# Performance work log

Measured on AMD Instinct MI355X. Metric: run time of the kernel, lower is better.

Reference implementation:

```python
import jax, jax.numpy as jnp
import numpy as np

B = 65536

def setup_inputs() -> dict:
    key = jax.random.key(0)
    ks = jax.random.split(key, 6)
    x = jax.random.normal(ks[0], (B, 784), dtype=jnp.float32)
    w_conv = jnp.ones((3, 3), dtype=jnp.float32)  # Parameter(ones((3,3)))
    w1 = jax.random.normal(ks[1], (676, 256), dtype=jnp.float32) * 0.04
    b1 = jax.random.normal(ks[2], (256,), dtype=jnp.float32) * 0.01
    w2 = jax.random.normal(ks[3], (256, 10), dtype=jnp.float32) * 0.06
    b2 = jax.random.normal(ks[4], (10,), dtype=jnp.float32) * 0.01
    return {"x": x, "w_conv": w_conv, "w1": w1, "b1": b1, "w2": w2, "b2": b2}

def reference(x, w_conv, w1, b1, w2, b2):
    b = x.shape[0]
    img = x.reshape(b, 1, 28, 28)
    # Convolve() is cross-correlation (no kernel flip), 'VALID': 28->26
    kern = w_conv.reshape(1, 1, 3, 3)
    conv = jax.lax.conv_general_dilated(
        img, kern, window_strides=(1, 1), padding='VALID',
        dimension_numbers=('NCHW', 'OIHW', 'NCHW'))  # (B,1,26,26)
    feat = conv.reshape(b, 676)
    h = jax.nn.relu(feat @ w1 + b1)  # (B,256)
    return h @ w2 + b2               # (B,10)
```

## Files before the change

kernel.cpp:

```cpp
#include <hip/hip_runtime.h>
#include <hip/hip_bf16.h>
#include <stdint.h>

typedef __bf16 bf16;
typedef __attribute__((ext_vector_type(8))) __bf16 bf16x8;
typedef __attribute__((ext_vector_type(4))) float f32x4;

#define KREAL 784
#define NTILES 25
#define TROW   40
#define TILE_ELEMS (256 * TROW)

#define GLOBAL_AS __attribute__((address_space(1)))
#define LDS_AS    __attribute__((address_space(3)))

__global__ __launch_bounds__(256) void prep_w1tt(const float* __restrict__ w_conv,
                                                 const float* __restrict__ w1,
                                                 bf16* __restrict__ W) {
    const int tile = blockIdx.x / TROW;
    const int kk   = blockIdx.x % TROW;
    const int n    = threadIdx.x;
    const int k    = tile * 32 + kk;
    float s = 0.0f;
    if (kk < 32 && k < KREAL) {
        const int r = k / 28, c = k % 28;
        #pragma unroll
        for (int di = 0; di < 3; ++di) {
            const int i = r - di;
            if (i < 0 || i >= 26) continue;
            #pragma unroll
            for (int dj = 0; dj < 3; ++dj) {
                const int j = c - dj;
                if (j < 0 || j >= 26) continue;
                s += w_conv[di * 3 + dj] * w1[(i * 26 + j) * 256 + n];
            }
        }
    }
    W[(size_t)tile * TILE_ELEMS + n * TROW + kk] = (bf16)s;
}

__global__ __launch_bounds__(256, 2) void fused_mlp(
    const float* __restrict__ x,
    const bf16*  __restrict__ W,
    const float* __restrict__ b1,
    const float* __restrict__ w2,
    const float* __restrict__ b2,
    float* __restrict__ out)
{
    __shared__ bf16 Bs[3][TILE_ELEMS];

    const int t    = threadIdx.x;
    const int wave = t >> 6;
    const int lane = t & 63;
    const int c    = lane & 15;
    const int q    = lane >> 4;

    const int row0 = blockIdx.x * 128;

    const float* arow0 = x + (size_t)(row0 + wave * 32 + c) * KREAL + q * 8;
    const float* arow1 = arow0 + (size_t)16 * KREAL;
    const bf16* bsrc = W + (size_t)(wave * 5) * 512 + lane * 8;

    f32x4 acc[2][16];
    #pragma unroll
    for (int mt = 0; mt < 2; ++mt)
        #pragma unroll
        for (int nt = 0; nt < 16; ++nt)
            acc[mt][nt] = (f32x4){0.f, 0.f, 0.f, 0.f};

    float4 f0a = *(const float4*)arow0, f0b = *(const float4*)(arow0 + 4);
    float4 f1a = *(const float4*)arow1, f1b = *(const float4*)(arow1 + 4);
    #pragma unroll
    for (int j = 0; j < 5; ++j) {
        __builtin_amdgcn_global_load_lds(
            (const GLOBAL_AS void*)(bsrc + j * 512),
            (LDS_AS void*)((char*)&Bs[0][0] + (wave * 5 + j) * 1024), 16, 0, 0);
    }
    #pragma unroll
    for (int j = 0; j < 5; ++j) {
        __builtin_amdgcn_global_load_lds(
            (const GLOBAL_AS void*)(bsrc + TILE_ELEMS + j * 512),
            (LDS_AS void*)((char*)&Bs[1][0] + (wave * 5 + j) * 1024), 16, 0, 0);
    }
    bf16x8 a0, a1;
    a0[0] = (bf16)f0a.x; a0[1] = (bf16)f0a.y; a0[2] = (bf16)f0a.z; a0[3] = (bf16)f0a.w;
    a0[4] = (bf16)f0b.x; a0[5] = (bf16)f0b.y; a0[6] = (bf16)f0b.z; a0[7] = (bf16)f0b.w;
    a1[0] = (bf16)f1a.x; a1[1] = (bf16)f1a.y; a1[2] = (bf16)f1a.z; a1[3] = (bf16)f1a.w;
    a1[4] = (bf16)f1b.x; a1[5] = (bf16)f1b.y; a1[6] = (bf16)f1b.z; a1[7] = (bf16)f1b.w;

    asm volatile("s_waitcnt vmcnt(5)" ::: "memory");
    __builtin_amdgcn_sched_barrier(0);
    __builtin_amdgcn_s_barrier();
    __builtin_amdgcn_sched_barrier(0);

    #pragma unroll 1
    for (int it = 0; it < NTILES; ++it) {
        const int  cur   = it % 3;
        const bool more  = (it + 1) < NTILES;
        const bool more2 = (it + 2) < NTILES;

        float okm = 1.0f;
        if (more) {
            const int kn = (it + 1) * 32;
            const bool ok = (kn + q * 8) < KREAL;
            okm = ok ? 1.0f : 0.0f;
            const int koff = ok ? kn : 0;
            const float* p0 = arow0 + koff;
            const float* p1 = arow1 + koff;
            f0a = *(const float4*)p0; f0b = *(const float4*)(p0 + 4);
            f1a = *(const float4*)p1; f1b = *(const float4*)(p1 + 4);
        }

        if (more2) {
            const bf16* bs = bsrc + (size_t)(it + 2) * TILE_ELEMS;
            char* bd = (char*)&Bs[(it + 2) % 3][0] + wave * 5 * 1024;
            #pragma unroll
            for (int j = 0; j < 5; ++j) {
                __builtin_amdgcn_global_load_lds(
                    (const GLOBAL_AS void*)(bs + j * 512),
                    (LDS_AS void*)(bd + j * 1024), 16, 0, 0);
            }
        }

        {
            const bf16* bb = &Bs[cur][0] + c * TROW + q * 8;
            #pragma unroll
            for (int nt = 0; nt < 16; ++nt) {
                bf16x8 b = *(const bf16x8*)(bb + nt * 16 * TROW);
                acc[0][nt] = __builtin_amdgcn_mfma_f32_16x16x32_bf16(a0, b, acc[0][nt], 0, 0, 0);
                acc[1][nt] = __builtin_amdgcn_mfma_f32_16x16x32_bf16(a1, b, acc[1][nt], 0, 0, 0);
            }
        }

        if (more) {
            a0[0] = (bf16)(f0a.x * okm); a0[1] = (bf16)(f0a.y * okm);
            a0[2] = (bf16)(f0a.z * okm); a0[3] = (bf16)(f0a.w * okm);
            a0[4] = (bf16)(f0b.x * okm); a0[5] = (bf16)(f0b.y * okm);
            a0[6] = (bf16)(f0b.z * okm); a0[7] = (bf16)(f0b.w * okm);
            a1[0] = (bf16)(f1a.x * okm); a1[1] = (bf16)(f1a.y * okm);
            a1[2] = (bf16)(f1a.z * okm); a1[3] = (bf16)(f1a.w * okm);
            a1[4] = (bf16)(f1b.x * okm); a1[5] = (bf16)(f1b.y * okm);
            a1[6] = (bf16)(f1b.z * okm); a1[7] = (bf16)(f1b.w * okm);
        }

        if (more) {
            if (more2) {
                asm volatile("s_waitcnt vmcnt(5)" ::: "memory");
            } else {
                asm volatile("s_waitcnt vmcnt(0)" ::: "memory");
            }
            __builtin_amdgcn_sched_barrier(0);
            __builtin_amdgcn_s_barrier();
            __builtin_amdgcn_sched_barrier(0);
        }
    }

    float bl[16];
    #pragma unroll
    for (int nt = 0; nt < 16; ++nt) bl[nt] = b1[nt * 16 + c];

    #pragma unroll
    for (int mt = 0; mt < 2; ++mt)
        #pragma unroll
        for (int nt = 0; nt < 16; ++nt)
            #pragma unroll
            for (int r = 0; r < 4; ++r) {
                float v = acc[mt][nt][r] + bl[nt];
                acc[mt][nt][r] = v > 0.f ? v : 0.f;
            }

    #pragma unroll 1
    for (int j = 0; j < 10; ++j) {
        float wj[16];
        #pragma unroll
        for (int nt = 0; nt < 16; ++nt) wj[nt] = w2[(nt * 16 + c) * 10 + j];
        const float b2j = b2[j];
        #pragma unroll
        for (int mt = 0; mt < 2; ++mt)
            #pragma unroll
            for (int r = 0; r < 4; ++r) {
                float s = 0.f;
                #pragma unroll
                for (int nt = 0; nt < 16; ++nt) s += acc[mt][nt][r] * wj[nt];
                s += __shfl_xor(s, 1, 64);
                s += __shfl_xor(s, 2, 64);
                s += __shfl_xor(s, 4, 64);
                s += __shfl_xor(s, 8, 64);
                if (c == j) {
                    const int row = row0 + wave * 32 + mt * 16 + q * 4 + r;
                    out[(size_t)row * 10 + j] = s + b2j;
                }
            }
    }
}

extern "C" void kernel_launch(void* const* d_in, const int* in_sizes, int n_in,
                              void* d_out, int out_size, void* d_ws, size_t ws_size,
                              hipStream_t stream) {
    const float* x  = (const float*)d_in[0];
    const float* wc = (const float*)d_in[1];
    const float* w1 = (const float*)d_in[2];
    const float* b1 = (const float*)d_in[3];
    const float* w2 = (const float*)d_in[4];
    const float* b2 = (const float*)d_in[5];
    float* out = (float*)d_out;
    bf16* W = (bf16*)d_ws;

    prep_w1tt<<<dim3(NTILES * TROW), dim3(256), 0, stream>>>(wc, w1, W);
    fused_mlp<<<dim3(65536 / 128), dim3(256), 0, stream>>>(x, W, b1, w2, b2, out);
}
```

Before: 324.6 us.

## Halve rows per block and switch to double-buffered weight tiles for occupancy

Each wave now computes 16 rows instead of 32, so the block tile shrinks from 128 to 64 rows and the grid doubles. The weight staging in LDS drops from triple to double buffering, with a full vmcnt(0) wait each iteration. Launch bounds rise to 4 blocks per SM, aiming to hide x-load latency through occupancy. The cost is that each weight tile read from LDS and global memory now feeds half as many MFMAs, and prefetch depth is reduced.

```diff
diff --git a/kernel.cpp b/kernel.cpp
--- a/kernel.cpp
+++ b/kernel.cpp
@@ -39,7 +39,7 @@
     W[(size_t)tile * TILE_ELEMS + n * TROW + kk] = (bf16)s;
 }
 
-__global__ __launch_bounds__(256, 2) void fused_mlp(
+__global__ __launch_bounds__(256, 4) void fused_mlp(
     const float* __restrict__ x,
     const bf16*  __restrict__ W,
     const float* __restrict__ b1,
@@ -47,7 +47,7 @@
     const float* __restrict__ b2,
     float* __restrict__ out)
 {
-    __shared__ bf16 Bs[3][TILE_ELEMS];
+    __shared__ bf16 Bs[2][TILE_ELEMS];
 
     const int t    = threadIdx.x;
     const int wave = t >> 6;
@@ -55,49 +55,36 @@
     const int c    = lane & 15;
     const int q    = lane >> 4;
 
-    const int row0 = blockIdx.x * 128;
+    const int row0 = blockIdx.x * 64;
 
-    const float* arow0 = x + (size_t)(row0 + wave * 32 + c) * KREAL + q * 8;
-    const float* arow1 = arow0 + (size_t)16 * KREAL;
+    const float* arow0 = x + (size_t)(row0 + wave * 16 + c) * KREAL + q * 8;
     const bf16* bsrc = W + (size_t)(wave * 5) * 512 + lane * 8;
 
-    f32x4 acc[2][16];
+    f32x4 acc[16];
     #pragma unroll
-    for (int mt = 0; mt < 2; ++mt)
-        #pragma unroll
-        for (int nt = 0; nt < 16; ++nt)
-            acc[mt][nt] = (f32x4){0.f, 0.f, 0.f, 0.f};
+    for (int nt = 0; nt < 16; ++nt)
+        acc[nt] = (f32x4){0.f, 0.f, 0.f, 0.f};
 
     float4 f0a = *(const float4*)arow0, f0b = *(const float4*)(arow0 + 4);
-    float4 f1a = *(const float4*)arow1, f1b = *(const float4*)(arow1 + 4);
     #pragma unroll
     for (int j = 0; j < 5; ++j) {
         __builtin_amdgcn_global_load_lds(
             (const GLOBAL_AS void*)(bsrc + j * 512),
             (LDS_AS void*)((char*)&Bs[0][0] + (wave * 5 + j) * 1024), 16, 0, 0);
     }
-    #pragma unroll
-    for (int j = 0; j < 5; ++j) {
-        __builtin_amdgcn_global_load_lds(
-            (const GLOBAL_AS void*)(bsrc + TILE_ELEMS + j * 512),
-            (LDS_AS void*)((char*)&Bs[1][0] + (wave * 5 + j) * 1024), 16, 0, 0);
-    }
-    bf16x8 a0, a1;
+    bf16x8 a0;
     a0[0] = (bf16)f0a.x; a0[1] = (bf16)f0a.y; a0[2] = (bf16)f0a.z; a0[3] = (bf16)f0a.w;
     a0[4] = (bf16)f0b.x; a0[5] = (bf16)f0b.y; a0[6] = (bf16)f0b.z; a0[7] = (bf16)f0b.w;
-    a1[0] = (bf16)f1a.x; a1[1] = (bf16)f1a.y; a1[2] = (bf16)f1a.z; a1[3] = (bf16)f1a.w;
-    a1[4] = (bf16)f1b.x; a1[5] = (bf16)f1b.y; a1[6] = (bf16)f1b.z; a1[7] = (bf16)f1b.w;
 
-    asm volatile("s_waitcnt vmcnt(5)" ::: "memory");
+    asm volatile("s_waitcnt vmcnt(0)" ::: "memory");
     __builtin_amdgcn_sched_barrier(0);
     __builtin_amdgcn_s_barrier();
     __builtin_amdgcn_sched_barrier(0);
 
     #pragma unroll 1
     for (int it = 0; it < NTILES; ++it) {
-        const int  cur   = it % 3;
-        const bool more  = (it + 1) < NTILES;
-        const bool more2 = (it + 2) < NTILES;
+        const int  cur  = it & 1;
+        const bool more = (it + 1) < NTILES;
 
         float okm = 1.0f;
         if (more) {
@@ -106,14 +93,12 @@
             okm = ok ? 1.0f : 0.0f;
             const int koff = ok ? kn : 0;
             const float* p0 = arow0 + koff;
-            const float* p1 = arow1 + koff;
             f0a = *(const float4*)p0; f0b = *(const float4*)(p0 + 4);
-            f1a = *(const float4*)p1; f1b = *(const float4*)(p1 + 4);
         }
 
-        if (more2) {
-            const bf16* bs = bsrc + (size_t)(it + 2) * TILE_ELEMS;
-            char* bd = (char*)&Bs[(it + 2) % 3][0] + wave * 5 * 1024;
+        if (more) {
+            const bf16* bs = bsrc + (size_t)(it + 1) * TILE_ELEMS;
+            char* bd = (char*)&Bs[cur ^ 1][0] + wave * 5 * 1024;
             #pragma unroll
             for (int j = 0; j < 5; ++j) {
                 __builtin_amdgcn_global_load_lds(
@@ -127,8 +112,7 @@
             #pragma unroll
             for (int nt = 0; nt < 16; ++nt) {
                 bf16x8 b = *(const bf16x8*)(bb + nt * 16 * TROW);
-                acc[0][nt] = __builtin_amdgcn_mfma_f32_16x16x32_bf16(a0, b, acc[0][nt], 0, 0, 0);
-                acc[1][nt] = __builtin_amdgcn_mfma_f32_16x16x32_bf16(a1, b, acc[1][nt], 0, 0, 0);
+                acc[nt] = __builtin_amdgcn_mfma_f32_16x16x32_bf16(a0, b, acc[nt], 0, 0, 0);
             }
         }
 
@@ -137,18 +121,10 @@
             a0[2] = (bf16)(f0a.z * okm); a0[3] = (bf16)(f0a.w * okm);
             a0[4] = (bf16)(f0b.x * okm); a0[5] = (bf16)(f0b.y * okm);
             a0[6] = (bf16)(f0b.z * okm); a0[7] = (bf16)(f0b.w * okm);
-            a1[0] = (bf16)(f1a.x * okm); a1[1] = (bf16)(f1a.y * okm);
-            a1[2] = (bf16)(f1a.z * okm); a1[3] = (bf16)(f1a.w * okm);
-            a1[4] = (bf16)(f1b.x * okm); a1[5] = (bf16)(f1b.y * okm);
-            a1[6] = (bf16)(f1b.z * okm); a1[7] = (bf16)(f1b.w * okm);
         }
 
         if (more) {
-            if (more2) {
-                asm volatile("s_waitcnt vmcnt(5)" ::: "memory");
-            } else {
-                asm volatile("s_waitcnt vmcnt(0)" ::: "memory");
-            }
+            asm volatile("s_waitcnt vmcnt(0)" ::: "memory");
             __builtin_amdgcn_sched_barrier(0);
             __builtin_amdgcn_s_barrier();
             __builtin_amdgcn_sched_barrier(0);
@@ -160,14 +136,12 @@
     for (int nt = 0; nt < 16; ++nt) bl[nt] = b1[nt * 16 + c];
 
     #pragma unroll
-    for (int mt = 0; mt < 2; ++mt)
+    for (int nt = 0; nt < 16; ++nt)
         #pragma unroll
-        for (int nt = 0; nt < 16; ++nt)
-            #pragma unroll
-            for (int r = 0; r < 4; ++r) {
-                float v = acc[mt][nt][r] + bl[nt];
-                acc[mt][nt][r] = v > 0.f ? v : 0.f;
-            }
+        for (int r = 0; r < 4; ++r) {
+            float v = acc[nt][r] + bl[nt];
+            acc[nt][r] = v > 0.f ? v : 0.f;
+        }
 
     #pragma unroll 1
     for (int j = 0; j < 10; ++j) {
@@ -176,21 +150,19 @@
         for (int nt = 0; nt < 16; ++nt) wj[nt] = w2[(nt * 16 + c) * 10 + j];
         const float b2j = b2[j];
         #pragma unroll
-        for (int mt = 0; mt < 2; ++mt)
+        for (int r = 0; r < 4; ++r) {
+            float s = 0.f;
             #pragma unroll
-            for (int r = 0; r < 4; ++r) {
-                float s = 0.f;
-                #pragma unroll
-                for (int nt = 0; nt < 16; ++nt) s += acc[mt][nt][r] * wj[nt];
-                s += __shfl_xor(s, 1, 64);
-                s += __shfl_xor(s, 2, 64);
-                s += __shfl_xor(s, 4, 64);
-                s += __shfl_xor(s, 8, 64);
-                if (c == j) {
-                    const int row = row0 + wave * 32 + mt * 16 + q * 4 + r;
-                    out[(size_t)row * 10 + j] = s + b2j;
-                }
+            for (int nt = 0; nt < 16; ++nt) s += acc[nt][r] * wj[nt];
+            s += __shfl_xor(s, 1, 64);
+            s += __shfl_xor(s, 2, 64);
+            s += __shfl_xor(s, 4, 64);
+            s += __shfl_xor(s, 8, 64);
+            if (c == j) {
+                const int row = row0 + wave * 16 + q * 4 + r;
+                out[(size_t)row * 10 + j] = s + b2j;
             }
+        }
     }
 }
 
@@ -207,5 +179,5 @@
     bf16* W = (bf16*)d_ws;
 
     prep_w1tt<<<dim3(NTILES * TROW), dim3(256), 0, stream>>>(wc, w1, W);
-    fused_mlp<<<dim3(65536 / 128), dim3(256), 0, stream>>>(x, W, b1, w2, b2, out);
+    fused_mlp<<<dim3(65536 / 64), dim3(256), 0, stream>>>(x, W, b1, w2, b2, out);
 }
```

New measurement: 340.6 us. +4.9%, slower.
